# Optimization experiments

Hardware: AMD Instinct MI355X
Metric: run time of the kernel (lower is better)

## Reference

```python
import jax, jax.numpy as jnp
import numpy as np

NEG_INF = -1e30  # large negative in place of -inf for masked scores (fp32-safe)


def setup_inputs() -> dict:
    key = jax.random.key(0)
    kq, kk, kv, km = jax.random.split(key, 4)
    B, H, S, D = 2, 16, 2048, 64
    query = jax.random.normal(kq, (B, H, S, D), dtype=jnp.float32)
    k = jax.random.normal(kk, (B, H, S, D), dtype=jnp.float32)
    v = jax.random.normal(kv, (B, H, S, D), dtype=jnp.float32)
    mask = jax.random.randint(km, (B, H, S, S), 0, 2, dtype=jnp.int32)
    return {"query": query, "key": k, "value": v, "mask": mask}


def reference(query, key, value, mask):
    # Online-softmax chunked attention is mathematically exact softmax attention;
    # we compute the equivalent masked softmax attention in one fused expression.
    d_k = query.shape[-1]
    scale = 1.0 / np.sqrt(d_k).astype(np.float32)
    # scores: [B, H, Sq, Sk]
    scores = jnp.einsum('bhqd,bhkd->bhqk', query, key) * scale
    scores = jnp.where(mask == 0, NEG_INF, scores)
    attn = jax.nn.softmax(scores, axis=-1)
    out = jnp.einsum('bhqk,bhkd->bhqd', attn, value)
    return out
```

## Files before the change

### kernel.cpp

```cpp
#include <hip/hip_runtime.h>


typedef __attribute__((ext_vector_type(8))) short bf16x8;
typedef __attribute__((ext_vector_type(4))) float f32x4;

#define S_LEN 2048
#define D_DIM 64
#define NT 32
#define PP 72

__device__ __forceinline__ short f2bf(float f) {
    union { float f; unsigned u; } v; v.f = f;
    unsigned r = v.u + 0x7fffu + ((v.u >> 16) & 1u);
    return (short)(r >> 16);
}

__device__ __forceinline__ bf16x8 cvt8(float4 a, float4 b, float s) {
    bf16x8 f;
    f[0]=f2bf(a.x*s); f[1]=f2bf(a.y*s); f[2]=f2bf(a.z*s); f[3]=f2bf(a.w*s);
    f[4]=f2bf(b.x*s); f[5]=f2bf(b.y*s); f[6]=f2bf(b.z*s); f[7]=f2bf(b.w*s);
    return f;
}

__global__ __launch_bounds__(256)
void pack_q(const float* __restrict__ Q, short* __restrict__ Qw) {
    const int bh = blockIdx.x, qt = blockIdx.y;
    for (int ci = threadIdx.x; ci < 512; ci += 256) {
        int w = ci >> 7, ks = (ci >> 6) & 1, lane = ci & 63;
        int quad = lane >> 4, c = lane & 15;
        int row = qt * 64 + w * 16 + c;
        int d0 = ks * 32 + quad * 8;
        const float* src = Q + ((size_t)(bh * S_LEN + row)) * D_DIM + d0;
        float4 a = *(const float4*)src;
        float4 b = *(const float4*)(src + 4);
        *(bf16x8*)(Qw + ((size_t)(bh * 32 + qt) * 512 + ci) * 8) = cvt8(a, b, 0.125f);
    }
}

__global__ __launch_bounds__(256)
void pack_k(const float* __restrict__ K, short* __restrict__ Kw) {
    const int bh = blockIdx.x, t = blockIdx.y;
    for (int ci = threadIdx.x; ci < 512; ci += 256) {
        int fb = ci >> 6, lane = ci & 63;
        int nb = fb >> 1, ks = fb & 1;
        int quad = lane >> 4, c = lane & 15;
        int key = t * 64 + c * 4 + nb;
        int d0 = ks * 32 + quad * 8;
        const float* src = K + ((size_t)(bh * S_LEN + key)) * D_DIM + d0;
        float4 a = *(const float4*)src;
        float4 b = *(const float4*)(src + 4);
        *(bf16x8*)(Kw + ((size_t)(bh * 32 + t) * 512 + ci) * 8) = cvt8(a, b, 1.0f);
    }
}

__global__ __launch_bounds__(256)
void pack_v(const float* __restrict__ V, short* __restrict__ Vw) {
    __shared__ float vt[64][65];
    const int bh = blockIdx.x, t = blockIdx.y;
    {
        int key = threadIdx.x >> 2, d0 = (threadIdx.x & 3) * 16;
        const float* src = V + ((size_t)(bh * S_LEN + t * 64 + key)) * D_DIM + d0;
        float4 a = *(const float4*)src;
        float4 b = *(const float4*)(src + 4);
        float4 cc = *(const float4*)(src + 8);
        float4 d = *(const float4*)(src + 12);
        float* dst = &vt[key][d0];
        dst[0]=a.x; dst[1]=a.y; dst[2]=a.z; dst[3]=a.w;
        dst[4]=b.x; dst[5]=b.y; dst[6]=b.z; dst[7]=b.w;
        dst[8]=cc.x; dst[9]=cc.y; dst[10]=cc.z; dst[11]=cc.w;
        dst[12]=d.x; dst[13]=d.y; dst[14]=d.z; dst[15]=d.w;
    }
    __syncthreads();
    for (int ci = threadIdx.x; ci < 512; ci += 256) {
        int fb = ci >> 6, lane = ci & 63;
        int db = fb >> 1, ks = fb & 1;
        int quad = lane >> 4, c = lane & 15;
        bf16x8 f;
#pragma unroll
        for (int j = 0; j < 8; ++j) {
            int pos = ks * 32 + quad * 8 + j;
            int kin = (pos & 15) * 4 + (pos >> 4);
            f[j] = f2bf(vt[kin][db * 16 + c]);
        }
        *(bf16x8*)(Vw + ((size_t)(bh * 32 + t) * 512 + ci) * 8) = f;
    }
}

typedef __attribute__((address_space(3))) unsigned lds_u32;
typedef const __attribute__((address_space(1))) unsigned glob_u32;

__global__ __launch_bounds__(256, 3)
void fa_main(const short* __restrict__ Qw, const short* __restrict__ Kw,
             const short* __restrict__ Vw, const int* __restrict__ M,
             float* __restrict__ O) {
    __shared__ __align__(16) short KVb[2 * 16 * 512];
    __shared__ __align__(16) short Pwv[4 * 16 * PP];

    const int tid  = threadIdx.x;
    const int lane = tid & 63;
    const int w    = tid >> 6;
    const int quad = lane >> 4;
    const int c    = lane & 15;

    const int bid = blockIdx.x;
    const int x = bid & 7, y = bid >> 3;
    const int bh = x * 4 + (y >> 5);
    const int qt = y & 31;

    const short* qbase = Qw + ((size_t)(bh * 32 + qt) * 512 + w * 128 + lane) * 8;
    const bf16x8 qf0 = *(const bf16x8*)qbase;
    const bf16x8 qf1 = *(const bf16x8*)(qbase + 64 * 8);

    const short* gkv = (w < 2) ? (Kw + (size_t)bh * 32 * 4096)
                               : (Vw + (size_t)bh * 32 * 4096);
    const int fb0 = (w & 1) * 4;
    const int vofs = (w < 2) ? 0 : 4096;

    const int* mrow = M + ((size_t)(bh * S_LEN + qt * 64 + w * 16 + quad * 4)) * S_LEN + 4 * c;

    f32x4 acco[4];
    float lacc[4];
#pragma unroll
    for (int r = 0; r < 4; ++r) {
        lacc[r] = 0.f;
        acco[r][0]=0.f; acco[r][1]=0.f; acco[r][2]=0.f; acco[r][3]=0.f;
    }

#pragma unroll
    for (int i = 0; i < 4; ++i) {
        const short* src = gkv + (size_t)(fb0 + i) * 512 + lane * 8;
        short* dst = &KVb[vofs + (fb0 + i) * 512];
        __builtin_amdgcn_global_load_lds((glob_u32*)src, (lds_u32*)dst, 16, 0, 0);
    }
    int4 mcur[4];
#pragma unroll
    for (int r = 0; r < 4; ++r) mcur[r] = *(const int4*)(mrow + (size_t)r * S_LEN);
    __syncthreads();

    short* pw = &Pwv[w * 16 * PP];

    for (int t = 0; t < NT; ++t) {
        const int cur = (t & 1) * 8192, nxt = 8192 - cur;
        const int tn = (t + 1 < NT) ? t + 1 : 0;

#pragma unroll
        for (int i = 0; i < 4; ++i) {
            const short* src = gkv + (size_t)tn * 4096 + (fb0 + i) * 512 + lane * 8;
            short* dst = &KVb[nxt + vofs + (fb0 + i) * 512];
            __builtin_amdgcn_global_load_lds((glob_u32*)src, (lds_u32*)dst, 16, 0, 0);
        }
        int4 mnxt[4];
#pragma unroll
        for (int r = 0; r < 4; ++r)
            mnxt[r] = *(const int4*)(mrow + (size_t)r * S_LEN + tn * 64);

        f32x4 accs[4];
#pragma unroll
        for (int nb = 0; nb < 4; ++nb) { accs[nb][0]=0.f; accs[nb][1]=0.f; accs[nb][2]=0.f; accs[nb][3]=0.f; }
#pragma unroll
        for (int nb = 0; nb < 4; ++nb) {
            bf16x8 b0 = *(const bf16x8*)&KVb[cur + (nb * 2 + 0) * 512 + lane * 8];
            accs[nb] = __builtin_amdgcn_mfma_f32_16x16x32_bf16(qf0, b0, accs[nb], 0, 0, 0);
            bf16x8 b1 = *(const bf16x8*)&KVb[cur + (nb * 2 + 1) * 512 + lane * 8];
            accs[nb] = __builtin_amdgcn_mfma_f32_16x16x32_bf16(qf1, b1, accs[nb], 0, 0, 0);
        }

        float p[4][4];
#pragma unroll
        for (int r = 0; r < 4; ++r) {
            const int mm[4] = { mcur[r].x, mcur[r].y, mcur[r].z, mcur[r].w };
#pragma unroll
            for (int nb = 0; nb < 4; ++nb) {
                float e = __expf(accs[nb][r]);
                p[r][nb] = (mm[nb] != 0) ? e : 0.f;
            }
            lacc[r] += (p[r][0] + p[r][1]) + (p[r][2] + p[r][3]);
        }

#pragma unroll
        for (int r = 0; r < 4; ++r)
#pragma unroll
            for (int nb = 0; nb < 4; ++nb)
                pw[(quad * 4 + r) * PP + nb * 16 + c] = f2bf(p[r][nb]);
        bf16x8 pf0 = *(const bf16x8*)&pw[c * PP + quad * 8];
        bf16x8 pf1 = *(const bf16x8*)&pw[c * PP + 32 + quad * 8];

#pragma unroll
        for (int db = 0; db < 4; ++db) {
            bf16x8 v0 = *(const bf16x8*)&KVb[cur + 4096 + (db * 2 + 0) * 512 + lane * 8];
            acco[db] = __builtin_amdgcn_mfma_f32_16x16x32_bf16(pf0, v0, acco[db], 0, 0, 0);
            bf16x8 v1 = *(const bf16x8*)&KVb[cur + 4096 + (db * 2 + 1) * 512 + lane * 8];
            acco[db] = __builtin_amdgcn_mfma_f32_16x16x32_bf16(pf1, v1, acco[db], 0, 0, 0);
        }

#pragma unroll
        for (int r = 0; r < 4; ++r) mcur[r] = mnxt[r];
        __syncthreads();
    }

    float* orow = O + ((size_t)(bh * S_LEN + qt * 64 + w * 16 + quad * 4)) * D_DIM + c;
#pragma unroll
    for (int r = 0; r < 4; ++r) {
        float l = lacc[r];
        l += __shfl_xor(l, 1);
        l += __shfl_xor(l, 2);
        l += __shfl_xor(l, 4);
        l += __shfl_xor(l, 8);
        float inv = 1.0f / l;
#pragma unroll
        for (int db = 0; db < 4; ++db)
            orow[(size_t)r * D_DIM + db * 16] = acco[db][r] * inv;
    }
}

extern "C" void kernel_launch(void* const* d_in, const int* in_sizes, int n_in,
                              void* d_out, int out_size, void* d_ws, size_t ws_size,
                              hipStream_t stream) {
    const float* Q = (const float*)d_in[0];
    const float* K = (const float*)d_in[1];
    const float* V = (const float*)d_in[2];
    const int*   M = (const int*)d_in[3];
    float* O = (float*)d_out;

    short* Qw = (short*)d_ws;
    short* Kw = Qw + (size_t)32 * 32 * 4096;
    short* Vw = Kw + (size_t)32 * 32 * 4096;

    hipLaunchKernelGGL(pack_q, dim3(32, 32), dim3(256), 0, stream, Q, Qw);
    hipLaunchKernelGGL(pack_k, dim3(32, 32), dim3(256), 0, stream, K, Kw);
    hipLaunchKernelGGL(pack_v, dim3(32, 32), dim3(256), 0, stream, V, Vw);
    hipLaunchKernelGGL(fa_main, dim3(1024), dim3(256), 0, stream, Qw, Kw, Vw, M, O);
}
```

Measured before the change: 780.4 us.

## Merge pack kernels, software-pipeline PV behind QK, use exp2 with prescaled Q

Merges the three packing kernels into one launch indexed by blockIdx.z, which removes two launches. The main loop is restructured so the P·V MFMA for the previous tile runs alongside the Q·K MFMA for the current tile. K and V get separate double buffers, with V loaded one tile later than K. Q is prescaled by log2(e)/8 so the softmax can use the hardware exp2, and P is written to shared memory as packed 4-wide stores. The main kernel has no max subtraction, so exp of large scores may overflow, as it could before. Pipelining also raises register pressure under the occupancy-3 launch bound.

```diff
diff --git a/kernel.cpp b/kernel.cpp
--- a/kernel.cpp
+++ b/kernel.cpp
@@ -2,17 +2,26 @@
 
 
 typedef __attribute__((ext_vector_type(8))) short bf16x8;
+typedef __attribute__((ext_vector_type(4))) short s16x4;
 typedef __attribute__((ext_vector_type(4))) float f32x4;
 
 #define S_LEN 2048
-#define D_DIM 64
 #define NT 32
 #define PP 72
+#define QSCALE 0.1803368801f
 
 __device__ __forceinline__ short f2bf(float f) {
     union { float f; unsigned u; } v; v.f = f;
     unsigned r = v.u + 0x7fffu + ((v.u >> 16) & 1u);
     return (short)(r >> 16);
+}
+
+__device__ __forceinline__ float fexp2(float x) {
+#if __has_builtin(__builtin_amdgcn_exp2f)
+    return __builtin_amdgcn_exp2f(x);
+#else
+    return exp2f(x);
+#endif
 }
 
 __device__ __forceinline__ bf16x8 cvt8(float4 a, float4 b, float s) {
@@ -23,66 +32,61 @@
 }
 
 __global__ __launch_bounds__(256)
-void pack_q(const float* __restrict__ Q, short* __restrict__ Qw) {
-    const int bh = blockIdx.x, qt = blockIdx.y;
-    for (int ci = threadIdx.x; ci < 512; ci += 256) {
-        int w = ci >> 7, ks = (ci >> 6) & 1, lane = ci & 63;
-        int quad = lane >> 4, c = lane & 15;
-        int row = qt * 64 + w * 16 + c;
-        int d0 = ks * 32 + quad * 8;
-        const float* src = Q + ((size_t)(bh * S_LEN + row)) * D_DIM + d0;
-        float4 a = *(const float4*)src;
-        float4 b = *(const float4*)(src + 4);
-        *(bf16x8*)(Qw + ((size_t)(bh * 32 + qt) * 512 + ci) * 8) = cvt8(a, b, 0.125f);
-    }
-}
-
-__global__ __launch_bounds__(256)
-void pack_k(const float* __restrict__ K, short* __restrict__ Kw) {
-    const int bh = blockIdx.x, t = blockIdx.y;
-    for (int ci = threadIdx.x; ci < 512; ci += 256) {
-        int fb = ci >> 6, lane = ci & 63;
-        int nb = fb >> 1, ks = fb & 1;
-        int quad = lane >> 4, c = lane & 15;
-        int key = t * 64 + c * 4 + nb;
-        int d0 = ks * 32 + quad * 8;
-        const float* src = K + ((size_t)(bh * S_LEN + key)) * D_DIM + d0;
-        float4 a = *(const float4*)src;
-        float4 b = *(const float4*)(src + 4);
-        *(bf16x8*)(Kw + ((size_t)(bh * 32 + t) * 512 + ci) * 8) = cvt8(a, b, 1.0f);
-    }
-}
-
-__global__ __launch_bounds__(256)
-void pack_v(const float* __restrict__ V, short* __restrict__ Vw) {
+void pack_all(const float* __restrict__ Q, const float* __restrict__ K,
+              const float* __restrict__ V, short* __restrict__ Qw,
+              short* __restrict__ Kw, short* __restrict__ Vw) {
     __shared__ float vt[64][65];
-    const int bh = blockIdx.x, t = blockIdx.y;
-    {
-        int key = threadIdx.x >> 2, d0 = (threadIdx.x & 3) * 16;
-        const float* src = V + ((size_t)(bh * S_LEN + t * 64 + key)) * D_DIM + d0;
-        float4 a = *(const float4*)src;
-        float4 b = *(const float4*)(src + 4);
-        float4 cc = *(const float4*)(src + 8);
-        float4 d = *(const float4*)(src + 12);
-        float* dst = &vt[key][d0];
-        dst[0]=a.x; dst[1]=a.y; dst[2]=a.z; dst[3]=a.w;
-        dst[4]=b.x; dst[5]=b.y; dst[6]=b.z; dst[7]=b.w;
-        dst[8]=cc.x; dst[9]=cc.y; dst[10]=cc.z; dst[11]=cc.w;
-        dst[12]=d.x; dst[13]=d.y; dst[14]=d.z; dst[15]=d.w;
-    }
-    __syncthreads();
-    for (int ci = threadIdx.x; ci < 512; ci += 256) {
-        int fb = ci >> 6, lane = ci & 63;
-        int db = fb >> 1, ks = fb & 1;
-        int quad = lane >> 4, c = lane & 15;
-        bf16x8 f;
-#pragma unroll
-        for (int j = 0; j < 8; ++j) {
-            int pos = ks * 32 + quad * 8 + j;
-            int kin = (pos & 15) * 4 + (pos >> 4);
-            f[j] = f2bf(vt[kin][db * 16 + c]);
-        }
-        *(bf16x8*)(Vw + ((size_t)(bh * 32 + t) * 512 + ci) * 8) = f;
+    const int bh = blockIdx.x, t = blockIdx.y, which = blockIdx.z;
+    if (which == 0) {
+        for (int ci = threadIdx.x; ci < 512; ci += 256) {
+            int ww = ci >> 7, ks = (ci >> 6) & 1, lane = ci & 63;
+            int quad = lane >> 4, c = lane & 15;
+            int row = t * 64 + ww * 16 + c;
+            int d0 = ks * 32 + quad * 8;
+            const float* src = Q + ((size_t)(bh * S_LEN + row)) * 64 + d0;
+            float4 a = *(const float4*)src;
+            float4 b = *(const float4*)(src + 4);
+            *(bf16x8*)(Qw + ((size_t)(bh * 32 + t) * 512 + ci) * 8) = cvt8(a, b, QSCALE);
+        }
+    } else if (which == 1) {
+        for (int ci = threadIdx.x; ci < 512; ci += 256) {
+            int fb = ci >> 6, lane = ci & 63;
+            int nb = fb >> 1, ks = fb & 1;
+            int quad = lane >> 4, c = lane & 15;
+            int key = t * 64 + c * 4 + nb;
+            int d0 = ks * 32 + quad * 8;
+            const float* src = K + ((size_t)(bh * S_LEN + key)) * 64 + d0;
+            float4 a = *(const float4*)src;
+            float4 b = *(const float4*)(src + 4);
+            *(bf16x8*)(Kw + ((size_t)(bh * 32 + t) * 512 + ci) * 8) = cvt8(a, b, 1.0f);
+        }
+    } else {
+        {
+            int key = threadIdx.x >> 2, d0 = (threadIdx.x & 3) * 16;
+            const float* src = V + ((size_t)(bh * S_LEN + t * 64 + key)) * 64 + d0;
+            float4 a = *(const float4*)src;
+            float4 b = *(const float4*)(src + 4);
+            float4 cc = *(const float4*)(src + 8);
+            float4 d = *(const float4*)(src + 12);
+            float* dst = &vt[key][d0];
+            dst[0]=a.x; dst[1]=a.y; dst[2]=a.z; dst[3]=a.w;
+            dst[4]=b.x; dst[5]=b.y; dst[6]=b.z; dst[7]=b.w;
+            dst[8]=cc.x; dst[9]=cc.y; dst[10]=cc.z; dst[11]=cc.w;
+            dst[12]=d.x; dst[13]=d.y; dst[14]=d.z; dst[15]=d.w;
+        }
+        __syncthreads();
+        for (int ci = threadIdx.x; ci < 512; ci += 256) {
+            int fb = ci >> 6, lane = ci & 63;
+            int db = fb >> 1, ks = fb & 1;
+            int quad = lane >> 4, c = lane & 15;
+            bf16x8 f;
+#pragma unroll
+            for (int j = 0; j < 8; ++j) {
+                int pos = ks * 32 + quad * 8 + j;
+                f[j] = f2bf(vt[pos][db * 16 + c]);
+            }
+            *(bf16x8*)(Vw + ((size_t)(bh * 32 + t) * 512 + ci) * 8) = f;
+        }
     }
 }
 
@@ -93,7 +97,8 @@
 void fa_main(const short* __restrict__ Qw, const short* __restrict__ Kw,
              const short* __restrict__ Vw, const int* __restrict__ M,
              float* __restrict__ O) {
-    __shared__ __align__(16) short KVb[2 * 16 * 512];
+    __shared__ __align__(16) short Kb[2 * 8 * 512];
+    __shared__ __align__(16) short Vb[2 * 8 * 512];
     __shared__ __align__(16) short Pwv[4 * 16 * PP];
 
     const int tid  = threadIdx.x;
@@ -109,12 +114,11 @@
 
     const short* qbase = Qw + ((size_t)(bh * 32 + qt) * 512 + w * 128 + lane) * 8;
     const bf16x8 qf0 = *(const bf16x8*)qbase;
-    const bf16x8 qf1 = *(const bf16x8*)(qbase + 64 * 8);
-
-    const short* gkv = (w < 2) ? (Kw + (size_t)bh * 32 * 4096)
-                               : (Vw + (size_t)bh * 32 * 4096);
-    const int fb0 = (w & 1) * 4;
-    const int vofs = (w < 2) ? 0 : 4096;
+    const bf16x8 qf1 = *(const bf16x8*)(qbase + 512);
+
+    const bool isK = (w < 2);
+    const short* gsrc = (isK ? Kw : Vw) + (size_t)bh * 32 * 4096 + (w & 1) * 2048 + (size_t)lane * 8;
+    short* ldst0 = (isK ? Kb : Vb) + (w & 1) * 2048;
 
     const int* mrow = M + ((size_t)(bh * S_LEN + qt * 64 + w * 16 + quad * 4)) * S_LEN + 4 * c;
 
@@ -126,11 +130,11 @@
         acco[r][0]=0.f; acco[r][1]=0.f; acco[r][2]=0.f; acco[r][3]=0.f;
     }
 
-#pragma unroll
-    for (int i = 0; i < 4; ++i) {
-        const short* src = gkv + (size_t)(fb0 + i) * 512 + lane * 8;
-        short* dst = &KVb[vofs + (fb0 + i) * 512];
-        __builtin_amdgcn_global_load_lds((glob_u32*)src, (lds_u32*)dst, 16, 0, 0);
+    if (isK) {
+#pragma unroll
+        for (int i = 0; i < 4; ++i)
+            __builtin_amdgcn_global_load_lds((glob_u32*)(gsrc + i * 512),
+                                             (lds_u32*)(ldst0 + i * 512), 16, 0, 0);
     }
     int4 mcur[4];
 #pragma unroll
@@ -138,67 +142,77 @@
     __syncthreads();
 
     short* pw = &Pwv[w * 16 * PP];
-
+    const short* pr = &Pwv[w * 16 * PP + c * PP];
+
+#pragma unroll 2
     for (int t = 0; t < NT; ++t) {
-        const int cur = (t & 1) * 8192, nxt = 8192 - cur;
-        const int tn = (t + 1 < NT) ? t + 1 : 0;
-
-#pragma unroll
-        for (int i = 0; i < 4; ++i) {
-            const short* src = gkv + (size_t)tn * 4096 + (fb0 + i) * 512 + lane * 8;
-            short* dst = &KVb[nxt + vofs + (fb0 + i) * 512];
-            __builtin_amdgcn_global_load_lds((glob_u32*)src, (lds_u32*)dst, 16, 0, 0);
-        }
+        const int tn = (t + 1) & (NT - 1);
+        const int dtile = isK ? tn : t;
+        const int dbuf = (dtile & 1) * 4096;
+#pragma unroll
+        for (int i = 0; i < 4; ++i)
+            __builtin_amdgcn_global_load_lds((glob_u32*)(gsrc + (size_t)dtile * 4096 + i * 512),
+                                             (lds_u32*)(ldst0 + dbuf + i * 512), 16, 0, 0);
         int4 mnxt[4];
 #pragma unroll
         for (int r = 0; r < 4; ++r)
             mnxt[r] = *(const int4*)(mrow + (size_t)r * S_LEN + tn * 64);
 
+        const int kc = (t & 1) * 4096;
         f32x4 accs[4];
 #pragma unroll
         for (int nb = 0; nb < 4; ++nb) { accs[nb][0]=0.f; accs[nb][1]=0.f; accs[nb][2]=0.f; accs[nb][3]=0.f; }
 #pragma unroll
         for (int nb = 0; nb < 4; ++nb) {
-            bf16x8 b0 = *(const bf16x8*)&KVb[cur + (nb * 2 + 0) * 512 + lane * 8];
+            bf16x8 b0 = *(const bf16x8*)&Kb[kc + (nb * 2 + 0) * 512 + lane * 8];
             accs[nb] = __builtin_amdgcn_mfma_f32_16x16x32_bf16(qf0, b0, accs[nb], 0, 0, 0);
-            bf16x8 b1 = *(const bf16x8*)&KVb[cur + (nb * 2 + 1) * 512 + lane * 8];
+            bf16x8 b1 = *(const bf16x8*)&Kb[kc + (nb * 2 + 1) * 512 + lane * 8];
             accs[nb] = __builtin_amdgcn_mfma_f32_16x16x32_bf16(qf1, b1, accs[nb], 0, 0, 0);
         }
 
-        float p[4][4];
+        if (t > 0) {
+            const int vc = ((t - 1) & 1) * 4096;
+            bf16x8 pf0 = *(const bf16x8*)(pr + quad * 8);
+            bf16x8 pf1 = *(const bf16x8*)(pr + 32 + quad * 8);
+#pragma unroll
+            for (int db = 0; db < 4; ++db) {
+                bf16x8 v0 = *(const bf16x8*)&Vb[vc + (db * 2 + 0) * 512 + lane * 8];
+                acco[db] = __builtin_amdgcn_mfma_f32_16x16x32_bf16(pf0, v0, acco[db], 0, 0, 0);
+                bf16x8 v1 = *(const bf16x8*)&Vb[vc + (db * 2 + 1) * 512 + lane * 8];
+                acco[db] = __builtin_amdgcn_mfma_f32_16x16x32_bf16(pf1, v1, acco[db], 0, 0, 0);
+            }
+        }
+
 #pragma unroll
         for (int r = 0; r < 4; ++r) {
-            const int mm[4] = { mcur[r].x, mcur[r].y, mcur[r].z, mcur[r].w };
-#pragma unroll
-            for (int nb = 0; nb < 4; ++nb) {
-                float e = __expf(accs[nb][r]);
-                p[r][nb] = (mm[nb] != 0) ? e : 0.f;
-            }
-            lacc[r] += (p[r][0] + p[r][1]) + (p[r][2] + p[r][3]);
-        }
-
-#pragma unroll
-        for (int r = 0; r < 4; ++r)
-#pragma unroll
-            for (int nb = 0; nb < 4; ++nb)
-                pw[(quad * 4 + r) * PP + nb * 16 + c] = f2bf(p[r][nb]);
-        bf16x8 pf0 = *(const bf16x8*)&pw[c * PP + quad * 8];
-        bf16x8 pf1 = *(const bf16x8*)&pw[c * PP + 32 + quad * 8];
-
-#pragma unroll
-        for (int db = 0; db < 4; ++db) {
-            bf16x8 v0 = *(const bf16x8*)&KVb[cur + 4096 + (db * 2 + 0) * 512 + lane * 8];
-            acco[db] = __builtin_amdgcn_mfma_f32_16x16x32_bf16(pf0, v0, acco[db], 0, 0, 0);
-            bf16x8 v1 = *(const bf16x8*)&KVb[cur + 4096 + (db * 2 + 1) * 512 + lane * 8];
-            acco[db] = __builtin_amdgcn_mfma_f32_16x16x32_bf16(pf1, v1, acco[db], 0, 0, 0);
-        }
-
+            const int4 mm = mcur[r];
+            float e0 = fexp2(accs[0][r]); e0 = (mm.x != 0) ? e0 : 0.f;
+            float e1 = fexp2(accs[1][r]); e1 = (mm.y != 0) ? e1 : 0.f;
+            float e2 = fexp2(accs[2][r]); e2 = (mm.z != 0) ? e2 : 0.f;
+            float e3 = fexp2(accs[3][r]); e3 = (mm.w != 0) ? e3 : 0.f;
+            lacc[r] += (e0 + e1) + (e2 + e3);
+            s16x4 pk = { f2bf(e0), f2bf(e1), f2bf(e2), f2bf(e3) };
+            *(s16x4*)&pw[(quad * 4 + r) * PP + 4 * c] = pk;
+        }
 #pragma unroll
         for (int r = 0; r < 4; ++r) mcur[r] = mnxt[r];
         __syncthreads();
     }
 
-    float* orow = O + ((size_t)(bh * S_LEN + qt * 64 + w * 16 + quad * 4)) * D_DIM + c;
+    {
+        const int vc = ((NT - 1) & 1) * 4096;
+        bf16x8 pf0 = *(const bf16x8*)(pr + quad * 8);
+        bf16x8 pf1 = *(const bf16x8*)(pr + 32 + quad * 8);
+#pragma unroll
+        for (int db = 0; db < 4; ++db) {
+            bf16x8 v0 = *(const bf16x8*)&Vb[vc + (db * 2 + 0) * 512 + lane * 8];
+            acco[db] = __builtin_amdgcn_mfma_f32_16x16x32_bf16(pf0, v0, acco[db], 0, 0, 0);
+            bf16x8 v1 = *(const bf16x8*)&Vb[vc + (db * 2 + 1) * 512 + lane * 8];
+            acco[db] = __builtin_amdgcn_mfma_f32_16x16x32_bf16(pf1, v1, acco[db], 0, 0, 0);
+        }
+    }
+
+    float* orow = O + ((size_t)(bh * S_LEN + qt * 64 + w * 16 + quad * 4)) * 64 + c;
 #pragma unroll
     for (int r = 0; r < 4; ++r) {
         float l = lacc[r];
@@ -209,7 +223,7 @@
         float inv = 1.0f / l;
 #pragma unroll
         for (int db = 0; db < 4; ++db)
-            orow[(size_t)r * D_DIM + db * 16] = acco[db][r] * inv;
+            orow[(size_t)r * 64 + db * 16] = acco[db][r] * inv;
     }
 }
 
@@ -226,8 +240,6 @@
     short* Kw = Qw + (size_t)32 * 32 * 4096;
     short* Vw = Kw + (size_t)32 * 32 * 4096;
 
-    hipLaunchKernelGGL(pack_q, dim3(32, 32), dim3(256), 0, stream, Q, Qw);
-    hipLaunchKernelGGL(pack_k, dim3(32, 32), dim3(256), 0, stream, K, Kw);
-    hipLaunchKernelGGL(pack_v, dim3(32, 32), dim3(256), 0, stream, V, Vw);
+    hipLaunchKernelGGL(pack_all, dim3(32, 32, 3), dim3(256), 0, stream, Q, K, V, Qw, Kw, Vw);
     hipLaunchKernelGGL(fa_main, dim3(1024), dim3(256), 0, stream, Qw, Kw, Vw, M, O);
 }
```

Measured after the change: 748.8 us. -4.0%, faster.
